# Kernel tuning notes

Measured on AMD Instinct MI355X. Metric: run time of the kernel, lower is better.

Reference implementation:

```python
import jax, jax.numpy as jnp
import numpy as np

N = 50000      # nodes
E = 1600000    # edges (avg degree 32)
IN = 4         # in_size
H = 64         # hidden size


def _gcn_conv(x, W, b, src, dst, ew, n):
    """PyG GCNConv with edge_weight: add self-loops (weight 1), symmetric
    deg^{-1/2} normalization, gather-transform-scatter aggregation, then bias."""
    xw = x @ W  # [n, out] transform first (PyG lin before propagate)
    loops = jnp.arange(n)
    s = jnp.concatenate([src, loops])
    d = jnp.concatenate([dst, loops])
    w = jnp.concatenate([ew, jnp.ones((n,), ew.dtype)])
    deg = jax.ops.segment_sum(w, d, num_segments=n)
    dinv = jnp.where(deg > 0, jax.lax.rsqrt(deg), 0.0)
    norm = dinv[s] * w * dinv[d]                      # [E+n]
    msg = xw[s] * norm[:, None]                       # [E+n, out]
    out = jax.ops.segment_sum(msg, d, num_segments=n)
    return out + b


def _tower(x, src, dst, ew, W0, b0, W1, b1, W2, b2, Wl, bl):
    # basic_gcn: GCNConv+ReLU, GCNConv+ReLU, GCNConv, then nn.Linear(out,out)
    n = x.shape[0]
    h = jax.nn.relu(_gcn_conv(x, W0, b0, src, dst, ew, n))
    h = jax.nn.relu(_gcn_conv(h, W1, b1, src, dst, ew, n))
    h = _gcn_conv(h, W2, b2, src, dst, ew, n)
    return h @ Wl + bl


def setup_inputs() -> dict:
    key = jax.random.key(0)
    ks = jax.random.split(key, 20)
    x = jax.random.normal(ks[0], (N, IN), dtype=jnp.float32)
    edge_index = jax.random.randint(ks[1], (2, E), 0, N, dtype=jnp.int64)
    edge_weights = jax.random.uniform(ks[2], (E,), dtype=jnp.float32)

    def lin(k, fin, fout):
        return jax.random.normal(k, (fin, fout), dtype=jnp.float32) * (1.0 / np.sqrt(fin))

    inp = {"x": x, "edge_index": edge_index, "edge_weights": edge_weights}
    # optim tower: in_size=4 -> 64 -> 64 -> 1, plus Linear(1,1)
    inp["o_W0"], inp["o_b0"] = lin(ks[3], IN, H), jnp.zeros((H,), jnp.float32)
    inp["o_W1"], inp["o_b1"] = lin(ks[4], H, H), jnp.zeros((H,), jnp.float32)
    inp["o_W2"], inp["o_b2"] = lin(ks[5], H, 1), jnp.zeros((1,), jnp.float32)
    inp["o_Wl"], inp["o_bl"] = lin(ks[6], 1, 1), jnp.zeros((1,), jnp.float32)
    # gamma tower: in_size+1=5 -> 64 -> 64 -> 1, plus Linear(1,1)
    inp["g_W0"], inp["g_b0"] = lin(ks[7], IN + 1, H), jnp.zeros((H,), jnp.float32)
    inp["g_W1"], inp["g_b1"] = lin(ks[8], H, H), jnp.zeros((H,), jnp.float32)
    inp["g_W2"], inp["g_b2"] = lin(ks[9], H, 1), jnp.zeros((1,), jnp.float32)
    inp["g_Wl"], inp["g_bl"] = lin(ks[10], 1, 1), jnp.zeros((1,), jnp.float32)
    return inp


def reference(x, edge_index, edge_weights,
              o_W0, o_b0, o_W1, o_b1, o_W2, o_b2, o_Wl, o_bl,
              g_W0, g_b0, g_W1, g_b1, g_W2, g_b2, g_Wl, g_bl):
    src, dst = edge_index[0], edge_index[1]
    # x_sol = optim tower (constraints=None -> no range scaling)
    x_sol = _tower(x, src, dst, edge_weights,
                   o_W0, o_b0, o_W1, o_b1, o_W2, o_b2, o_Wl, o_bl)  # [N,1]
    # gamma tower on cat(x, x_sol[:, -1:]); constraints=[0,1] -> sigmoid scaling
    xin = jnp.concatenate([x, x_sol[:, -1:]], axis=1)               # [N,5]
    g = _tower(xin, src, dst, edge_weights,
               g_W0, g_b0, g_W1, g_b1, g_W2, g_b2, g_Wl, g_bl)      # [N,1]
    gamma = jax.nn.sigmoid(g)  # scale_to_range(x, [0,1])
    # s == g == 1: gated residual combine
    x_new = x[:, -1:] + gamma * (x_sol - x[:, -1:])
    return (x_new, gamma)
```

## Files before the change

kernel.cpp:

```cpp
#include <hip/hip_runtime.h>
#include <hip/hip_fp16.h>
#include <math.h>

#define NN 50000
#define NE 1600000
#define NBK 196
#define EPB 4096
#define CAP 9216

typedef unsigned int u32;
typedef _Float16 f16x8 __attribute__((ext_vector_type(8)));
typedef float f32x4 __attribute__((ext_vector_type(4)));

static inline int cdiv(int a, int b){ return (a + b - 1) / b; }



__global__ void k_bucket(const int* __restrict__ src, const int* __restrict__ dst,
                         const float* __restrict__ ew, int* __restrict__ bcur,
                         int2* __restrict__ seL, int e){
  __shared__ int h[NBK], base[NBK], curL[NBK];
  int t = threadIdx.x;
  for (int b = t; b < NBK; b += 256){ h[b] = 0; curL[b] = 0; }
  __syncthreads();
  int beg = blockIdx.x*EPB;
  int d[16];
  #pragma unroll
  for (int i = 0; i < 16; ++i){
    int idx = beg + t + i*256;
    d[i] = (idx < e) ? dst[idx] : -1;
    if (d[i] >= 0) atomicAdd(&h[d[i] >> 8], 1);
  }
  __syncthreads();
  for (int b = t; b < NBK; b += 256)
    if (h[b] > 0) base[b] = b*CAP + atomicAdd(&bcur[b], h[b]);
  __syncthreads();
  #pragma unroll
  for (int i = 0; i < 16; ++i){
    int idx = beg + t + i*256;
    if (idx >= e) continue;
    int dd = d[i], b = dd >> 8;
    int pos = base[b] + atomicAdd(&curL[b], 1);
    seL[pos] = make_int2(((dd & 255) << 16) | src[idx], __float_as_int(ew[idx]));
  }
}

__global__ void k_csr_bucket(const int* __restrict__ bcur, const int2* __restrict__ seL,
                             const float* __restrict__ x, int* __restrict__ rowS,
                             int* __restrict__ rowE, u32* __restrict__ packed,
                             float* __restrict__ dinv, float* __restrict__ xd, int n){
  __shared__ int2 eb[CAP];
  __shared__ int hist[256], sh[256], cur[256];
  __shared__ float wsum[256];
  int b = blockIdx.x, t = threadIdx.x;
  int cnt = bcur[b];
  int ebeg = b*CAP;
  hist[t] = 0; wsum[t] = 0.f;
  __syncthreads();
  for (int i = t; i < cnt; i += 256){
    int2 u = seL[ebeg + i];
    eb[i] = u;
    int d = u.x >> 16;
    atomicAdd(&hist[d], 1);
    atomicAdd(&wsum[d], __int_as_float(u.y));
  }
  __syncthreads();
  int v = hist[t];
  sh[t] = v; __syncthreads();
  for (int o = 1; o < 256; o <<= 1){
    int u = (t >= o) ? sh[t-o] : 0;
    __syncthreads();
    sh[t] += u;
    __syncthreads();
  }
  int rs = ebeg + sh[t] - v;
  int node = b*256 + t;
  if (node < n){ rowS[node] = rs; rowE[node] = rs + v; }
  cur[t] = rs;
  __syncthreads();
  for (int i = t; i < cnt; i += 256){
    int2 u = eb[i];
    int d = u.x >> 16;
    int pos = atomicAdd(&cur[d], 1);
    packed[pos] = (u32)(u.x & 0xFFFF) |
                  ((u32)__half_as_ushort(__float2half(__int_as_float(u.y))) << 16);
  }
  __syncthreads();
  if (node < n){
    float di = rsqrtf(1.f + wsum[t]);
    dinv[node] = di;
    float4 xv = ((const float4*)x)[node];
    ((float4*)xd)[node] = make_float4(xv.x*di, xv.y*di, xv.z*di, xv.w*di);
  }
}


__global__ void k_agg4(const int* __restrict__ rowS, const int* __restrict__ rowE,
                       const u32* __restrict__ packed, const float* __restrict__ xd,
                       const float* __restrict__ dinv, float* __restrict__ y4, int n){
  int i = blockIdx.x*256 + threadIdx.x;
  if (i >= n) return;
  float4 self = ((const float4*)xd)[i];
  float ax = self.x, ay = self.y, az = self.z, aw = self.w;
  int end = rowE[i];
  for (int p = rowS[i]; p < end; ++p){
    u32 v = packed[p];
    float w = __half2float(__ushort_as_half((unsigned short)(v >> 16)));
    float4 xs = ((const float4*)xd)[v & 0xFFFF];
    ax = fmaf(w, xs.x, ax);
    ay = fmaf(w, xs.y, ay);
    az = fmaf(w, xs.z, az);
    aw = fmaf(w, xs.w, aw);
  }
  float di = dinv[i];
  ((float4*)y4)[i] = make_float4(ax*di, ay*di, az*di, aw*di);
}

template<int FIN>
__global__ __attribute__((amdgpu_waves_per_eu(2, 4)))
void k_conv2_mfma(const float* __restrict__ y4,
                  const int* __restrict__ rowS, const int* __restrict__ rowE,
                  const u32* __restrict__ packed, const float* __restrict__ xsolh,
                  const float* __restrict__ W0, const float* __restrict__ b0,
                  const float* __restrict__ W1, const float* __restrict__ dinv,
                  __half* __restrict__ out, int n){
  int lane = threadIdx.x & 63;
  int m = lane & 15, q = lane >> 4;
  int wid = (blockIdx.x*256 + threadIdx.x) >> 6;
  int nw = gridDim.x * 4;

  auto ldB = [&](int kk, int ct){
    f16x8 r;
    #pragma unroll
    for (int j = 0; j < 8; ++j)
      r[j] = (_Float16)W1[(kk*32 + q*8 + j)*64 + ct*16 + m];
    return r;
  };
  f16x8 b00 = ldB(0,0), b01 = ldB(0,1), b02 = ldB(0,2), b03 = ldB(0,3);
  f16x8 b10 = ldB(1,0), b11 = ldB(1,1), b12 = ldB(1,2), b13 = ldB(1,3);

  float w0c[2][FIN][8];
  float b0c[2][8];
  #pragma unroll
  for (int kk = 0; kk < 2; ++kk){
    #pragma unroll
    for (int j = 0; j < 8; ++j) b0c[kk][j] = b0[kk*32 + q*8 + j];
    #pragma unroll
    for (int c = 0; c < FIN; ++c)
      #pragma unroll
      for (int j = 0; j < 8; ++j)
        w0c[kk][c][j] = W0[c*64 + kk*32 + q*8 + j];
  }

  int ntiles = n >> 4;
  for (int tile = wid; tile < ntiles; tile += nw){
    int base = tile << 4;
    float4 yv = ((const float4*)y4)[base + m];
    float y5 = 0.f;
    if constexpr (FIN == 5){
      int node = base + m;
      int p0 = rowS[node] + q, end = rowE[node];
      float acc = 0.f;
      auto eproc = [&](int p){
        u32 v = (p < end) ? packed[p] : 0u;
        float w = __half2float(__ushort_as_half((unsigned short)(v >> 16)));
        acc = fmaf(w, xsolh[v & 0xFFFF], acc);
      };
      #pragma unroll
      for (int tt = 0; tt < 8; ++tt) eproc(p0 + 4*tt);
      if (p0 + 32 < end){
        #pragma unroll
        for (int tt = 8; tt < 16; ++tt) eproc(p0 + 4*tt);
      }
      for (int p = p0 + 64; p < end; p += 4) eproc(p);
      acc += __shfl_xor(acc, 16, 64);
      acc += __shfl_xor(acc, 32, 64);
      y5 = (acc + xsolh[node]) * dinv[node];
    }
    f16x8 a0, a1;
    #pragma unroll
    for (int j = 0; j < 8; ++j){
      float h0 = b0c[0][j], h1 = b0c[1][j];
      h0 = fmaf(yv.x, w0c[0][0][j], h0);  h1 = fmaf(yv.x, w0c[1][0][j], h1);
      h0 = fmaf(yv.y, w0c[0][1][j], h0);  h1 = fmaf(yv.y, w0c[1][1][j], h1);
      h0 = fmaf(yv.z, w0c[0][2][j], h0);  h1 = fmaf(yv.z, w0c[1][2][j], h1);
      h0 = fmaf(yv.w, w0c[0][3][j], h0);  h1 = fmaf(yv.w, w0c[1][3][j], h1);
      if constexpr (FIN == 5){
        h0 = fmaf(y5, w0c[0][4][j], h0);  h1 = fmaf(y5, w0c[1][4][j], h1);
      }
      a0[j] = (_Float16)fmaxf(h0, 0.f);
      a1[j] = (_Float16)fmaxf(h1, 0.f);
    }
    f32x4 c0 = {0,0,0,0}, c1 = {0,0,0,0}, c2 = {0,0,0,0}, c3 = {0,0,0,0};
    c0 = __builtin_amdgcn_mfma_f32_16x16x32_f16(a0, b00, c0, 0, 0, 0);
    c0 = __builtin_amdgcn_mfma_f32_16x16x32_f16(a1, b10, c0, 0, 0, 0);
    c1 = __builtin_amdgcn_mfma_f32_16x16x32_f16(a0, b01, c1, 0, 0, 0);
    c1 = __builtin_amdgcn_mfma_f32_16x16x32_f16(a1, b11, c1, 0, 0, 0);
    c2 = __builtin_amdgcn_mfma_f32_16x16x32_f16(a0, b02, c2, 0, 0, 0);
    c2 = __builtin_amdgcn_mfma_f32_16x16x32_f16(a1, b12, c2, 0, 0, 0);
    c3 = __builtin_amdgcn_mfma_f32_16x16x32_f16(a0, b03, c3, 0, 0, 0);
    c3 = __builtin_amdgcn_mfma_f32_16x16x32_f16(a1, b13, c3, 0, 0, 0);

    float4 dv = ((const float4*)dinv)[tile*4 + q];
    float dvr[4] = {dv.x, dv.y, dv.z, dv.w};
    auto st = [&](const f32x4& c, int ct){
      int ft = ct*16 + m;
      #pragma unroll
      for (int r = 0; r < 4; ++r)
        out[(size_t)(base + q*4 + r)*64 + ft] = __float2half(c[r]*dvr[r]);
    };
    st(c0, 0); st(c1, 1); st(c2, 2); st(c3, 3);
  }
}

__global__ __attribute__((amdgpu_waves_per_eu(4, 8)))
void k_agg64f(const int* __restrict__ rowS, const int* __restrict__ rowE,
              const u32* __restrict__ packed, const __half* __restrict__ xw,
              const float* __restrict__ dinv, const float* __restrict__ b,
              const float* __restrict__ W2, float* __restrict__ shat, int n){
  int tid = blockIdx.x*256 + threadIdx.x;
  int node = tid >> 6, lane = tid & 63;
  if (node >= n) return;
  int f2 = lane & 31, ep = lane >> 5;
  const __half2* xw2 = (const __half2*)xw;
  float ax = 0.f, ay = 0.f;
  int p = rowS[node], end = rowE[node];

  auto proc = [&](u32 myv, int t){
    u32 v0 = __builtin_amdgcn_readlane(myv, 2*t);
    u32 v1 = __builtin_amdgcn_readlane(myv, 2*t + 1);
    u32 v = ep ? v1 : v0;
    int s = v & 0xFFFF;
    float w = __half2float(__ushort_as_half((unsigned short)(v >> 16)));
    float2 xf = __half22float2(xw2[s*32 + f2]);
    ax = fmaf(w, xf.x, ax);
    ay = fmaf(w, xf.y, ay);
  };

  for (; p + 64 <= end; p += 64){
    u32 myv = __builtin_nontemporal_load(&packed[p + lane]);
    #pragma unroll
    for (int t = 0; t < 32; ++t) proc(myv, t);
  }
  int rem = end - p;
  if (rem > 0){
    u32 myv = (lane < rem) ? packed[p + lane] : 0u;
    #pragma unroll
    for (int t = 0; t < 16; ++t) proc(myv, t);
    if (rem > 32){
      #pragma unroll
      for (int t = 16; t < 32; ++t) proc(myv, t);
    }
  }

  ax += __shfl_xor(ax, 32, 64);
  ay += __shfl_xor(ay, 32, 64);
  float di = dinv[node];
  float2 sf = __half22float2(xw2[(size_t)node*32 + f2]);
  float hx = (ax + sf.x)*di + b[2*f2];
  float hy = (ay + sf.y)*di + b[2*f2 + 1];
  float2 w2 = ((const float2*)W2)[f2];
  float part = fmaxf(hx, 0.f)*w2.x + fmaxf(hy, 0.f)*w2.y;
  part += __shfl_xor(part, 16, 64);
  part += __shfl_xor(part, 8, 64);
  part += __shfl_xor(part, 4, 64);
  part += __shfl_xor(part, 2, 64);
  part += __shfl_xor(part, 1, 64);
  if (lane == 0) shat[node] = part * di;
}


__global__ void k_agg1_xsol(const int* __restrict__ rowS, const int* __restrict__ rowE,
                            const u32* __restrict__ packed, const float* __restrict__ shat,
                            const float* __restrict__ dinv, const float* __restrict__ b,
                            const float* __restrict__ Wl, const float* __restrict__ bl,
                            float* __restrict__ xsol, float* __restrict__ xsolh, int n){
  int tid = blockIdx.x*256 + threadIdx.x;
  int node = tid >> 5, l = tid & 31;
  if (node >= n) return;
  int beg = rowS[node], end = rowE[node];
  float acc = 0.f;
  for (int p = beg + l; p < end; p += 32){
    u32 v = packed[p];
    float w = __half2float(__ushort_as_half((unsigned short)(v >> 16)));
    acc = fmaf(w, shat[v & 0xFFFF], acc);
  }
  acc += __shfl_xor(acc, 16, 64);
  acc += __shfl_xor(acc, 8, 64);
  acc += __shfl_xor(acc, 4, 64);
  acc += __shfl_xor(acc, 2, 64);
  acc += __shfl_xor(acc, 1, 64);
  if (l == 0){
    float di = dinv[node];
    float h = (acc + shat[node])*di + b[0];
    float v = h*Wl[0] + bl[0];
    xsol[node]  = v;
    xsolh[node] = v*di;
  }
}

__global__ void k_agg1_final(const int* __restrict__ rowS, const int* __restrict__ rowE,
                             const u32* __restrict__ packed, const float* __restrict__ shat,
                             const float* __restrict__ dinv, const float* __restrict__ b,
                             const float* __restrict__ Wl, const float* __restrict__ bl,
                             const float* __restrict__ xsol, const float* __restrict__ x,
                             float* __restrict__ out, int n){
  int tid = blockIdx.x*256 + threadIdx.x;
  int node = tid >> 5, l = tid & 31;
  if (node >= n) return;
  int beg = rowS[node], end = rowE[node];
  float acc = 0.f;
  for (int p = beg + l; p < end; p += 32){
    u32 v = packed[p];
    float w = __half2float(__ushort_as_half((unsigned short)(v >> 16)));
    acc = fmaf(w, shat[v & 0xFFFF], acc);
  }
  acc += __shfl_xor(acc, 16, 64);
  acc += __shfl_xor(acc, 8, 64);
  acc += __shfl_xor(acc, 4, 64);
  acc += __shfl_xor(acc, 2, 64);
  acc += __shfl_xor(acc, 1, 64);
  if (l == 0){
    float di = dinv[node];
    float g = ((acc + shat[node])*di + b[0])*Wl[0] + bl[0];
    float gamma = 1.f / (1.f + expf(-g));
    float xl = x[node*4+3];
    out[node]     = xl + gamma*(xsol[node] - xl);
    out[n + node] = gamma;
  }
}


extern "C" void kernel_launch(void* const* d_in, const int* in_sizes, int n_in,
                              void* d_out, int out_size, void* d_ws, size_t ws_size,
                              hipStream_t stream){
  const float* x   = (const float*)d_in[0];
  const int*   ei  = (const int*)d_in[1];
  const float* ew  = (const float*)d_in[2];
  const float* oW0 = (const float*)d_in[3];
  const float* ob0 = (const float*)d_in[4];
  const float* oW1 = (const float*)d_in[5];
  const float* ob1 = (const float*)d_in[6];
  const float* oW2 = (const float*)d_in[7];
  const float* ob2 = (const float*)d_in[8];
  const float* oWl = (const float*)d_in[9];
  const float* obl = (const float*)d_in[10];
  const float* gW0 = (const float*)d_in[11];
  const float* gb0 = (const float*)d_in[12];
  const float* gW1 = (const float*)d_in[13];
  const float* gb1 = (const float*)d_in[14];
  const float* gW2 = (const float*)d_in[15];
  const float* gb2 = (const float*)d_in[16];
  const float* gWl = (const float*)d_in[17];
  const float* gbl = (const float*)d_in[18];

  const int n = NN, e = NE;
  const int* src = ei;
  const int* dst = ei + e;

  char* wsb = (char*)d_ws;
  int2*  seL    = (int2*)wsb;      wsb += (size_t)NBK*CAP*sizeof(int2);
  u32*   packed = (u32*)wsb;       wsb += (size_t)NBK*CAP*4;
  __half* bufA  = (__half*)wsb;    wsb += (size_t)n*64*2;
  float* y4     = (float*)wsb;     wsb += (size_t)n*4*4;
  float* xd     = (float*)wsb;     wsb += (size_t)n*4*4;
  int*   rowS   = (int*)wsb;       wsb += (size_t)n*4;
  int*   rowE   = (int*)wsb;       wsb += (size_t)n*4;
  int*   bcur   = (int*)wsb;       wsb += 256*4;
  float* dinv   = (float*)wsb;     wsb += (size_t)n*4;
  float* shat   = (float*)wsb;     wsb += (size_t)n*4;
  float* xsol   = (float*)wsb;     wsb += (size_t)n*4;
  float* xsolh  = (float*)wsb;     wsb += (size_t)n*4;

  dim3 b256(256);
  int gn  = cdiv(n, 256);
  int gw  = cdiv(n*64, 256);
  int gw2 = cdiv(n*32, 256);
  int gb  = cdiv(e, EPB);
  int gxm = 512;

  hipMemsetAsync(bcur, 0, 256*4, stream);
  k_bucket    <<<gb,  b256, 0, stream>>>(src, dst, ew, bcur, seL, e);
  k_csr_bucket<<<NBK, b256, 0, stream>>>(bcur, seL, x, rowS, rowE, packed, dinv, xd, n);

  k_agg4      <<<gn,  b256, 0, stream>>>(rowS, rowE, packed, xd, dinv, y4, n);

  k_conv2_mfma<4><<<gxm, b256, 0, stream>>>(y4, rowS, rowE, packed, nullptr,
                                            oW0, ob0, oW1, dinv, bufA, n);
  k_agg64f       <<<gw,  b256, 0, stream>>>(rowS, rowE, packed, bufA, dinv, ob1, oW2, shat, n);
  k_agg1_xsol    <<<gw2, b256, 0, stream>>>(rowS, rowE, packed, shat, dinv, ob2, oWl, obl, xsol, xsolh, n);

  k_conv2_mfma<5><<<gxm, b256, 0, stream>>>(y4, rowS, rowE, packed, xsolh,
                                            gW0, gb0, gW1, dinv, bufA, n);
  k_agg64f       <<<gw,  b256, 0, stream>>>(rowS, rowE, packed, bufA, dinv, gb1, gW2, shat, n);
  k_agg1_final   <<<gw2, b256, 0, stream>>>(rowS, rowE, packed, shat, dinv, gb2, gWl, gbl, xsol, x, (float*)d_out, n);
}
```

Measured before the change: 293.3 us.

## Split hidden features into two half-planes, lane-parallelize agg4, widen MFMA grid

The 64-wide fp16 hidden buffer is stored as two planes of 32 features, so each gather in the aggregation kernel reads a 64-byte row slice. Each wave now handles four edges at once with 16 lanes per edge instead of two edges with 32 lanes. The first 4-feature aggregation uses four lanes per node with an unrolled strided loop and a shuffle reduction, replacing one serial thread per node. The MFMA conv grid grows from 512 to 784 blocks. Trade-offs: more readlanes and reduction shuffles, and scattered fp16 stores into two planes.

```diff
diff --git a/kernel.cpp b/kernel.cpp
--- a/kernel.cpp
+++ b/kernel.cpp
@@ -98,22 +98,33 @@
 __global__ void k_agg4(const int* __restrict__ rowS, const int* __restrict__ rowE,
                        const u32* __restrict__ packed, const float* __restrict__ xd,
                        const float* __restrict__ dinv, float* __restrict__ y4, int n){
-  int i = blockIdx.x*256 + threadIdx.x;
-  if (i >= n) return;
-  float4 self = ((const float4*)xd)[i];
-  float ax = self.x, ay = self.y, az = self.z, aw = self.w;
-  int end = rowE[i];
-  for (int p = rowS[i]; p < end; ++p){
-    u32 v = packed[p];
+  int tid = blockIdx.x*256 + threadIdx.x;
+  int node = tid >> 2, l = tid & 3;
+  if (node >= n) return;
+  int p0 = rowS[node] + l, end = rowE[node];
+  float ax = 0.f, ay = 0.f, az = 0.f, aw = 0.f;
+  auto eproc = [&](int p){
+    u32 v = (p < end) ? packed[p] : 0u;
     float w = __half2float(__ushort_as_half((unsigned short)(v >> 16)));
     float4 xs = ((const float4*)xd)[v & 0xFFFF];
     ax = fmaf(w, xs.x, ax);
     ay = fmaf(w, xs.y, ay);
     az = fmaf(w, xs.z, az);
     aw = fmaf(w, xs.w, aw);
-  }
-  float di = dinv[i];
-  ((float4*)y4)[i] = make_float4(ax*di, ay*di, az*di, aw*di);
+  };
+  #pragma unroll
+  for (int t = 0; t < 12; ++t) eproc(p0 + 4*t);
+  for (int p = p0 + 48; p < end; p += 4) eproc(p);
+  ax += __shfl_xor(ax, 1, 64);  ax += __shfl_xor(ax, 2, 64);
+  ay += __shfl_xor(ay, 1, 64);  ay += __shfl_xor(ay, 2, 64);
+  az += __shfl_xor(az, 1, 64);  az += __shfl_xor(az, 2, 64);
+  aw += __shfl_xor(aw, 1, 64);  aw += __shfl_xor(aw, 2, 64);
+  if (l == 0){
+    float4 self = ((const float4*)xd)[node];
+    float di = dinv[node];
+    ((float4*)y4)[node] = make_float4((ax + self.x)*di, (ay + self.y)*di,
+                                      (az + self.z)*di, (aw + self.w)*di);
+  }
 }
 
 template<int FIN>
@@ -205,9 +216,10 @@
     float dvr[4] = {dv.x, dv.y, dv.z, dv.w};
     auto st = [&](const f32x4& c, int ct){
       int ft = ct*16 + m;
+      size_t hoff = (size_t)(ft >> 5)*(size_t)n*32 + (ft & 31);
       #pragma unroll
       for (int r = 0; r < 4; ++r)
-        out[(size_t)(base + q*4 + r)*64 + ft] = __float2half(c[r]*dvr[r]);
+        out[hoff + (size_t)(base + q*4 + r)*32] = __float2half(c[r]*dvr[r]);
     };
     st(c0, 0); st(c1, 1); st(c2, 2); st(c3, 3);
   }
@@ -221,47 +233,65 @@
   int tid = blockIdx.x*256 + threadIdx.x;
   int node = tid >> 6, lane = tid & 63;
   if (node >= n) return;
-  int f2 = lane & 31, ep = lane >> 5;
-  const __half2* xw2 = (const __half2*)xw;
-  float ax = 0.f, ay = 0.f;
+  int f2 = lane & 15, ep = lane >> 4;
+  const __half2* x0 = (const __half2*)xw;
+  const __half2* x1 = (const __half2*)(xw + (size_t)n*32);
+  float a0x = 0.f, a0y = 0.f, a1x = 0.f, a1y = 0.f;
   int p = rowS[node], end = rowE[node];
 
-  auto proc = [&](u32 myv, int t){
-    u32 v0 = __builtin_amdgcn_readlane(myv, 2*t);
-    u32 v1 = __builtin_amdgcn_readlane(myv, 2*t + 1);
-    u32 v = ep ? v1 : v0;
-    int s = v & 0xFFFF;
-    float w = __half2float(__ushort_as_half((unsigned short)(v >> 16)));
-    float2 xf = __half22float2(xw2[s*32 + f2]);
-    ax = fmaf(w, xf.x, ax);
-    ay = fmaf(w, xf.y, ay);
+  int ep1 = ep & 1, ep2 = ep & 2;
+  auto body = [&](u32 myv){
+    u32 vs[16];
+    #pragma unroll
+    for (int t = 0; t < 16; ++t){
+      u32 w0 = __builtin_amdgcn_readlane(myv, 4*t);
+      u32 w1 = __builtin_amdgcn_readlane(myv, 4*t + 1);
+      u32 w2 = __builtin_amdgcn_readlane(myv, 4*t + 2);
+      u32 w3 = __builtin_amdgcn_readlane(myv, 4*t + 3);
+      u32 lo = ep1 ? w1 : w0;
+      u32 hi = ep1 ? w3 : w2;
+      vs[t] = ep2 ? hi : lo;
+    }
+    #pragma unroll
+    for (int t = 0; t < 16; ++t){
+      int s = vs[t] & 0xFFFF;
+      float w = __half2float(__ushort_as_half((unsigned short)(vs[t] >> 16)));
+      float2 xf = __half22float2(x0[s*16 + f2]);
+      a0x = fmaf(w, xf.x, a0x);
+      a0y = fmaf(w, xf.y, a0y);
+    }
+    #pragma unroll
+    for (int t = 0; t < 16; ++t){
+      int s = vs[t] & 0xFFFF;
+      float w = __half2float(__ushort_as_half((unsigned short)(vs[t] >> 16)));
+      float2 xf = __half22float2(x1[s*16 + f2]);
+      a1x = fmaf(w, xf.x, a1x);
+      a1y = fmaf(w, xf.y, a1y);
+    }
   };
 
-  for (; p + 64 <= end; p += 64){
-    u32 myv = __builtin_nontemporal_load(&packed[p + lane]);
-    #pragma unroll
-    for (int t = 0; t < 32; ++t) proc(myv, t);
-  }
+  for (; p + 64 <= end; p += 64)
+    body(__builtin_nontemporal_load(&packed[p + lane]));
   int rem = end - p;
-  if (rem > 0){
-    u32 myv = (lane < rem) ? packed[p + lane] : 0u;
-    #pragma unroll
-    for (int t = 0; t < 16; ++t) proc(myv, t);
-    if (rem > 32){
-      #pragma unroll
-      for (int t = 16; t < 32; ++t) proc(myv, t);
-    }
-  }
-
-  ax += __shfl_xor(ax, 32, 64);
-  ay += __shfl_xor(ay, 32, 64);
+  if (rem > 0)
+    body((lane < rem) ? packed[p + lane] : 0u);
+
+  a0x += __shfl_xor(a0x, 16, 64);  a0x += __shfl_xor(a0x, 32, 64);
+  a0y += __shfl_xor(a0y, 16, 64);  a0y += __shfl_xor(a0y, 32, 64);
+  a1x += __shfl_xor(a1x, 16, 64);  a1x += __shfl_xor(a1x, 32, 64);
+  a1y += __shfl_xor(a1y, 16, 64);  a1y += __shfl_xor(a1y, 32, 64);
+
   float di = dinv[node];
-  float2 sf = __half22float2(xw2[(size_t)node*32 + f2]);
-  float hx = (ax + sf.x)*di + b[2*f2];
-  float hy = (ay + sf.y)*di + b[2*f2 + 1];
-  float2 w2 = ((const float2*)W2)[f2];
-  float part = fmaxf(hx, 0.f)*w2.x + fmaxf(hy, 0.f)*w2.y;
-  part += __shfl_xor(part, 16, 64);
+  float2 s0 = __half22float2(x0[(size_t)node*16 + f2]);
+  float2 s1 = __half22float2(x1[(size_t)node*16 + f2]);
+  float h0x = (a0x + s0.x)*di + b[2*f2];
+  float h0y = (a0y + s0.y)*di + b[2*f2 + 1];
+  float h1x = (a1x + s1.x)*di + b[32 + 2*f2];
+  float h1y = (a1y + s1.y)*di + b[32 + 2*f2 + 1];
+  float2 wA = ((const float2*)W2)[f2];
+  float2 wB = ((const float2*)W2)[16 + f2];
+  float part = fmaxf(h0x, 0.f)*wA.x + fmaxf(h0y, 0.f)*wA.y
+             + fmaxf(h1x, 0.f)*wB.x + fmaxf(h1y, 0.f)*wB.y;
   part += __shfl_xor(part, 8, 64);
   part += __shfl_xor(part, 4, 64);
   part += __shfl_xor(part, 2, 64);
@@ -373,17 +403,17 @@
   float* xsolh  = (float*)wsb;     wsb += (size_t)n*4;
 
   dim3 b256(256);
-  int gn  = cdiv(n, 256);
   int gw  = cdiv(n*64, 256);
   int gw2 = cdiv(n*32, 256);
+  int gw4 = cdiv(n*4, 256);
   int gb  = cdiv(e, EPB);
-  int gxm = 512;
+  int gxm = 784;
 
   hipMemsetAsync(bcur, 0, 256*4, stream);
   k_bucket    <<<gb,  b256, 0, stream>>>(src, dst, ew, bcur, seL, e);
   k_csr_bucket<<<NBK, b256, 0, stream>>>(bcur, seL, x, rowS, rowE, packed, dinv, xd, n);
 
-  k_agg4      <<<gn,  b256, 0, stream>>>(rowS, rowE, packed, xd, dinv, y4, n);
+  k_agg4      <<<gw4, b256, 0, stream>>>(rowS, rowE, packed, xd, dinv, y4, n);
 
   k_conv2_mfma<4><<<gxm, b256, 0, stream>>>(y4, rowS, rowE, packed, nullptr,
                                             oW0, ob0, oW1, dinv, bufA, n);
```

Result: slower. 310.7 us (+5.9%).
